# Kernel tuning notes

Hardware: AMD Instinct MI355X
Metric: run time of the kernel (lower is better)

The kernel has to match this reference:

```python
import jax, jax.numpy as jnp
import numpy as np

N_NODES = 50000
N_EDGES = 1600000
IN_DIM = 128
HEADS = 4
HEAD_DIM = 32  # out_dim // heads
N_REL = 3
NEG_SLOPE = 0.2


def setup_inputs() -> dict:
    key = jax.random.key(0)
    ks = jax.random.split(key, 8)
    x = jax.random.normal(ks[0], (N_NODES, IN_DIM), dtype=jnp.float32)
    edge_index = jax.random.randint(ks[1], (2, N_EDGES), 0, N_NODES, dtype=jnp.int64)
    edge_type = jax.random.randint(ks[2], (N_EDGES,), 0, N_REL, dtype=jnp.int64)
    # per-relation GATConv params (PyG layout: lin weight, att_src, att_dst, bias)
    s = 1.0 / np.sqrt(IN_DIM)
    W = jax.random.normal(ks[3], (N_REL, IN_DIM, HEADS * HEAD_DIM), dtype=jnp.float32) * s
    att_src = jax.random.normal(ks[4], (N_REL, HEADS, HEAD_DIM), dtype=jnp.float32) * s
    att_dst = jax.random.normal(ks[5], (N_REL, HEADS, HEAD_DIM), dtype=jnp.float32) * s
    bias = jnp.zeros((N_REL, HEADS * HEAD_DIM), dtype=jnp.float32)
    rel_w = jnp.ones((N_REL,), dtype=jnp.float32)  # relation_weights param
    return {"x": x, "W": W, "att_src": att_src, "att_dst": att_dst,
            "bias": bias, "rel_w": rel_w,
            "edge_index": edge_index, "edge_type": edge_type}


def reference(x, W, att_src, att_dst, bias, rel_w, edge_index, edge_type):
    N = x.shape[0]
    NEG = jnp.float32(-1e9)
    # self loops (GATConv add_self_loops=True) appended; present in every relation
    self_idx = jnp.arange(N, dtype=edge_index.dtype)
    src = jnp.concatenate([edge_index[0], self_idx])  # [E+N]
    dst = jnp.concatenate([edge_index[1], self_idx])  # [E+N]
    weights = jax.nn.softmax(rel_w)
    out = jnp.zeros((N, HEADS * HEAD_DIM), dtype=x.dtype)
    for r in range(N_REL):
        h = (x @ W[r]).reshape(N, HEADS, HEAD_DIM)  # [N,H,C]
        a_s = jnp.einsum('nhc,hc->nh', h, att_src[r])
        a_d = jnp.einsum('nhc,hc->nh', h, att_dst[r])
        score = jax.nn.leaky_relu(a_s[src] + a_d[dst], NEG_SLOPE)  # [E+N,H]
        mask = jnp.concatenate([edge_type == r, jnp.ones((N,), dtype=bool)])
        score = jnp.where(mask[:, None], score, NEG)  # mask out other relations
        # segment softmax over incoming edges per destination node
        smax = jax.ops.segment_max(score, dst, num_segments=N)  # finite: self-loops
        ex = jnp.exp(score - smax[dst])
        denom = jax.ops.segment_sum(ex, dst, num_segments=N)
        alpha = ex / denom[dst]  # [E+N,H]
        msg = alpha[:, :, None] * h[src]  # [E+N,H,C]
        rel_out = jax.ops.segment_sum(msg, dst, num_segments=N).reshape(N, HEADS * HEAD_DIM)
        out = out + weights[r] * (rel_out + bias[r])
    return out
```

## Files before the change

### kernel.cpp

```cpp
#include <hip/hip_runtime.h>
#include <hip/hip_bf16.h>
#include <hip/hip_fp16.h>
#include <math.h>

#define IN_DIM 128
#define OUT_DIM 128
#define HEADS 4
#define HEAD_DIM 32
#define NREL 3
#define NEG_SLOPE 0.2f

#define CHUNK 4096
#define BUCK_SHIFT 7
#define DPB 128
#define KPB 384
#define CAPE 6144
#define CAPS (CAPE + 3*DPB)

typedef __attribute__((ext_vector_type(8))) short short8;
typedef __attribute__((ext_vector_type(4))) float f32x4;
typedef unsigned short u16;

static __device__ __forceinline__ float leaky(float x){ return fmaxf(x, NEG_SLOPE*x); }
static __device__ __forceinline__ unsigned bf16rn(float x){
  unsigned b = __float_as_uint(x);
  b += 0x7FFF + ((b>>16)&1u);
  return b>>16;
}
static __device__ __forceinline__ unsigned h2pack(float a, float b){
  union { __half h[2]; unsigned u; } p;
  p.h[0] = __float2half_rn(a); p.h[1] = __float2half_rn(b);
  return p.u;
}

__global__ __launch_bounds__(256) void k_wprep(
    const float* __restrict__ W, const float* __restrict__ att_s,
    const float* __restrict__ att_d, const float* __restrict__ rw,
    const float* __restrict__ bias, u16* __restrict__ WTall,
    float* __restrict__ smw, float* __restrict__ biasMix){
  const int r = blockIdx.x / 9;
  const int tile = blockIdx.x % 9;
  const int t = threadIdx.x;
  const float* Wr = W + (size_t)r*IN_DIM*OUT_DIM;
  u16* WT = WTall + (size_t)r*144*128;
  if (tile < 8){
    const int col0 = tile*16;
    for (int i=t; i<16*128; i+=256){
      int col = col0 + (i>>7), k = i&127;
      WT[col*128 + k] = (u16)bf16rn(Wr[k*128 + col]);
    }
    return;
  }
  if (t < 128){
    int k = t;
    for (int h=0; h<4; h++){
      float ss=0.f, sd=0.f;
      for (int c=0; c<32; c++){
        float w = Wr[k*128 + h*32 + c];
        ss = fmaf(w, att_s[(r*4+h)*32+c], ss);
        sd = fmaf(w, att_d[(r*4+h)*32+c], sd);
      }
      WT[(128+h)*128 + k] = (u16)bf16rn(ss);
      WT[(132+h)*128 + k] = (u16)bf16rn(sd);
    }
  }
  for (int i=t; i<8*128; i+=256) WT[136*128 + i] = 0;
  if (r == 0){
    float m = fmaxf(rw[0], fmaxf(rw[1], rw[2]));
    float e0=__expf(rw[0]-m), e1=__expf(rw[1]-m), e2=__expf(rw[2]-m);
    float inv = 1.f/(e0+e1+e2);
    if (t < 3) smw[t] = (t==0?e0:(t==1?e1:e2))*inv;
    if (t < 128)
      biasMix[t] = inv*(e0*bias[t] + e1*bias[OUT_DIM+t] + e2*bias[2*OUT_DIM+t]);
  }
}

__global__ __launch_bounds__(256) void k_gemmhist(
    const float* __restrict__ x, const u16* __restrict__ WTall,
    unsigned* __restrict__ hq, float* __restrict__ as_, float* __restrict__ ad_,
    const int* __restrict__ ei, int* __restrict__ histG,
    int N, int E, int NCHUNK, int NBUCK){
  __shared__ int h[512];
  const int t = threadIdx.x;

  if (blockIdx.x < (unsigned)NCHUNK){
    const int c = blockIdx.x;
    h[t] = 0; h[t+256] = 0; __syncthreads();
    const int* dstp = ei + E;
    const int base = c*CHUNK;
    #pragma unroll 4
    for (int it=0; it<CHUNK/256; ++it){
      int e = base + it*256 + t;
      if (e < E) atomicAdd(&h[dstp[e]>>BUCK_SHIFT], 1);
    }
    __syncthreads();
    for (int k=t; k<NBUCK; k+=256) histG[k*NCHUNK + c] = h[k];
    return;
  }

  const int w = t >> 6;
  const int l = t & 63;
  const int row0 = (blockIdx.x - NCHUNK)*128 + w*32;
  const int lg = l >> 4;
  const int lc = l & 15;

  short8 afrag[4][2];
  #pragma unroll
  for (int ks=0; ks<4; ks++){
    const int k0 = ks*32 + lg*8;
    #pragma unroll
    for (int rf=0; rf<2; rf++){
      int row = row0 + rf*16 + lc;
      float4 v0, v1;
      if (row < N){
        const float4* xp = (const float4*)(x + (size_t)row*IN_DIM + k0);
        v0 = xp[0]; v1 = xp[1];
      } else { v0 = float4{0.f,0.f,0.f,0.f}; v1 = v0; }
      union { short8 s; unsigned u[4]; } pa;
      pa.u[0] = bf16rn(v0.x) | (bf16rn(v0.y)<<16);
      pa.u[1] = bf16rn(v0.z) | (bf16rn(v0.w)<<16);
      pa.u[2] = bf16rn(v1.x) | (bf16rn(v1.y)<<16);
      pa.u[3] = bf16rn(v1.z) | (bf16rn(v1.w)<<16);
      afrag[ks][rf] = pa.s;
    }
  }

  for (int r=0; r<NREL; r++){
    const u16* WT = WTall + (size_t)r*144*128;
    f32x4 acc[2][9];
    #pragma unroll
    for (int rf=0; rf<2; rf++)
      #pragma unroll
      for (int cf=0; cf<9; cf++) acc[rf][cf] = (f32x4){0.f,0.f,0.f,0.f};

    #pragma unroll
    for (int ks=0; ks<4; ks++){
      const int k0 = ks*32 + lg*8;
      #pragma unroll
      for (int cf=0; cf<9; cf++){
        short8 b = *(const short8*)(WT + (size_t)(cf*16 + lc)*128 + k0);
        #pragma unroll
        for (int rf=0; rf<2; rf++)
          acc[rf][cf] = __builtin_amdgcn_mfma_f32_16x16x32_bf16(afrag[ks][rf], b, acc[rf][cf], 0, 0, 0);
      }
    }

    #pragma unroll
    for (int rf=0; rf<2; rf++){
      #pragma unroll
      for (int j=0; j<4; j++){
        int row = row0 + rf*16 + lg*4 + j;
        bool ok = (row < N);
        size_t nidx = (size_t)r*N + row;
        #pragma unroll
        for (int cf=0; cf<8; cf++){
          float v = acc[rf][cf][j];
          float pv = __shfl_xor(v, 1);
          if (ok && !(l&1))
            hq[nidx*64 + cf*8 + (lc>>1)] = bf16rn(v) | (bf16rn(pv)<<16);
        }
        float av = acc[rf][8][j];
        if (ok && lc < 4)       as_[nidx*4 + lc]     = av;
        else if (ok && lc < 8)  ad_[nidx*4 + (lc-4)] = av;
      }
    }
  }
}

__global__ __launch_bounds__(256) void k_scanSeg(const int* __restrict__ histG,
                        int* __restrict__ chunkOff, int* __restrict__ totalE, int NCHUNK){
  __shared__ int sh[512];
  __shared__ int ps[256];
  const int b = blockIdx.x, t = threadIdx.x;
  sh[t]     = (t     < NCHUNK) ? histG[b*NCHUNK + t]     : 0;
  sh[t+256] = (t+256 < NCHUNK) ? histG[b*NCHUNK + t+256] : 0;
  __syncthreads();
  int e0 = sh[2*t], pair = e0 + sh[2*t+1];
  ps[t] = pair; __syncthreads();
  int x = pair;
  for (int off=1; off<256; off<<=1){
    int y = (t>=off)?ps[t-off]:0; __syncthreads();
    x += y; ps[t] = x; __syncthreads();
  }
  int ex = x - pair;
  if (2*t   < NCHUNK) chunkOff[b*NCHUNK + 2*t]   = ex;
  if (2*t+1 < NCHUNK) chunkOff[b*NCHUNK + 2*t+1] = ex + e0;
  if (t == 255) totalE[b] = x;
}

__global__ __launch_bounds__(256) void k_part(const int* __restrict__ et, const int* __restrict__ ei,
                       const int* __restrict__ chunkOff, unsigned* __restrict__ payload,
                       int E, int NCHUNK, int NBUCK){
  __shared__ int cur[512];
  const int c = blockIdx.x, t = threadIdx.x;
  for (int k=t; k<NBUCK; k+=256) cur[k] = k*CAPE + chunkOff[k*NCHUNK + c];
  __syncthreads();
  const int* dstp = ei + E;
  const int base = c*CHUNK;
  #pragma unroll 4
  for (int it=0; it<CHUNK/256; ++it){
    int e = base + it*256 + t;
    if (e < E){
      int d = dstp[e];
      int s = ei[e];
      int r = et[e];
      int b = d >> BUCK_SHIFT;
      int pos = atomicAdd(&cur[b], 1);
      payload[pos] = (unsigned)((d & (DPB-1)) | (r<<7) | (s<<9));
    }
  }
}

__global__ __launch_bounds__(512) void k_csr(const unsigned* __restrict__ payload,
                     const int* __restrict__ totalE,
                     const float* __restrict__ as_, const float* __restrict__ ad_,
                     const float* __restrict__ smw,
                     int* __restrict__ offs, uint4* __restrict__ slot,
                     float4* __restrict__ ivg,
                     int E, int N, int NCHUNK, int NBUCK){
  __shared__ int cntA[KPB];
  __shared__ int cur[KPB];
  __shared__ float den[KPB*4];
  __shared__ float4 adl[KPB];
  __shared__ int ps[DPB];
  const int b = blockIdx.x, t = threadIdx.x;
  const int bs = b*CAPE;
  const int be = bs + totalE[b];
  const int outbase = b*CAPS;
  const int validD = min(N - b*DPB, DPB);

  for (int k=t; k<KPB; k+=512) cntA[k] = 0;
  for (int k=t; k<KPB*4; k+=512) den[k] = 0.f;
  for (int k=t; k<KPB; k+=512){
    int dl = k/3, r = k - dl*3;
    int d2 = b*DPB + dl;
    adl[k] = (d2 < N) ? ((const float4*)ad_)[(size_t)r*N + d2] : (float4){0,0,0,0};
  }
  __syncthreads();
  for (int i=bs+t; i<be; i+=512){
    unsigned p = payload[i];
    atomicAdd(&cntA[(int)(p&(DPB-1))*NREL + (int)((p>>7)&3u)], 1);
  }
  __syncthreads();
  const int dst = b*DPB + t;
  int c0=0,c1=0,c2=0,sum=0,o0=0,o1=0,o2=0,hs=0;
  if (t < DPB){
    hs = (dst < N) ? 1 : 0;
    c0 = cntA[3*t]   + hs;
    c1 = cntA[3*t+1] + hs;
    c2 = cntA[3*t+2] + hs;
    sum = c0+c1+c2;
    ps[t] = sum;
  }
  __syncthreads();
  int xsc = sum;
  for (int off=1; off<DPB; off<<=1){
    int y = (t < DPB && t >= off) ? ps[t-off] : 0;
    __syncthreads();
    if (t < DPB) { xsc += y; ps[t] = xsc; }
    __syncthreads();
  }
  if (t < DPB){
    int ex = xsc - sum;
    o0 = outbase + ex; o1 = o0 + c0; o2 = o1 + c1;
    offs[b*(KPB+1) + 3*t]   = o0;
    offs[b*(KPB+1) + 3*t+1] = o1;
    offs[b*(KPB+1) + 3*t+2] = o2;
    cur[3*t]   = (o0 - outbase) + hs;
    cur[3*t+1] = (o1 - outbase) + hs;
    cur[3*t+2] = (o2 - outbase) + hs;
  }
  if (t == 0) offs[b*(KPB+1) + KPB] = outbase + (be - bs) + 3*validD;
  __syncthreads();
  for (int i=bs+t; i<be; i+=512){
    unsigned p = payload[i];
    int dl = (int)(p&(DPB-1)), r = (int)((p>>7)&3u), s = (int)(p>>9);
    int lkey = dl*NREL + r;
    int pos = outbase + atomicAdd(&cur[lkey], 1);
    float4 a4 = ((const float4*)as_)[(size_t)r*N + s];
    float4 b4 = adl[lkey];
    float ex0 = __expf(leaky(a4.x+b4.x));
    float ex1 = __expf(leaky(a4.y+b4.y));
    float ex2 = __expf(leaky(a4.z+b4.z));
    float ex3 = __expf(leaky(a4.w+b4.w));
    slot[pos] = (uint4){ (unsigned)(s | (r<<16)), h2pack(ex0,ex1), h2pack(ex2,ex3), 0u };
    atomicAdd(&den[lkey*4+0], ex0); atomicAdd(&den[lkey*4+1], ex1);
    atomicAdd(&den[lkey*4+2], ex2); atomicAdd(&den[lkey*4+3], ex3);
  }
  __syncthreads();
  if (t < DPB && dst < N){
    int starts[3] = {o0, o1, o2};
    #pragma unroll
    for (int r=0; r<NREL; r++){
      int lkey = 3*t + r;
      float4 a4 = ((const float4*)as_)[(size_t)r*N + dst];
      float4 b4 = adl[lkey];
      float s0 = __expf(leaky(a4.x+b4.x));
      float s1 = __expf(leaky(a4.y+b4.y));
      float s2 = __expf(leaky(a4.z+b4.z));
      float s3 = __expf(leaky(a4.w+b4.w));
      float w = smw[r];
      float4 iv;
      iv.x = w/(den[lkey*4+0]+s0);
      iv.y = w/(den[lkey*4+1]+s1);
      iv.z = w/(den[lkey*4+2]+s2);
      iv.w = w/(den[lkey*4+3]+s3);
      ivg[dst*3 + r] = iv;
      slot[starts[r]] = (uint4){ (unsigned)(dst | (r<<16)), h2pack(s0,s1), h2pack(s2,s3), 0u };
    }
  }
}

__global__ __launch_bounds__(128) void k_segment(
    const int* __restrict__ offs, const uint4* __restrict__ slot,
    const unsigned* __restrict__ hq,
    const float4* __restrict__ ivg, const float* __restrict__ biasMix,
    float* __restrict__ out, int N){
  const int wave = threadIdx.x >> 6;
  const int lane = threadIdx.x & 63;
  const int dst  = blockIdx.x*2 + wave;
  if (dst >= N) return;
  const int g  = lane >> 3;
  const int l8 = lane & 7;
  const int h0 = l8 >> 2;

  const int bb = dst >> BUCK_SHIFT;
  const int lk = (dst & (DPB-1))*3;
  const int* ob = offs + (size_t)bb*(KPB+1);
  int beg = __builtin_amdgcn_readfirstlane(ob[lk]);
  int end = __builtin_amdgcn_readfirstlane(ob[lk+3]);

  float4 v0 = ivg[dst*3+0], v1 = ivg[dst*3+1], v2 = ivg[dst*3+2];
  float iA0 = h0 ? v0.y : v0.x, iB0 = h0 ? v0.w : v0.z;
  float iA1 = h0 ? v1.y : v1.x, iB1 = h0 ? v1.w : v1.z;
  float iA2 = h0 ? v2.y : v2.x, iB2 = h0 ? v2.w : v2.z;

  float acc0[8], acc1[8];
  #pragma unroll
  for (int q=0; q<8; q++){ acc0[q]=0.f; acc1[q]=0.f; }

  for (int i0=beg; i0<end; i0+=16){
    int i = i0 + g;
    int j = i + 8;
    bool vi = (i < end), vj = (j < end);
    uint4 rec1 = {0,0,0,0}, rec2 = {0,0,0,0};
    if (vi) rec1 = slot[i];
    if (vj) rec2 = slot[j];
    uint4 u0a, u1a, u0b, u1b;
    if (vi){
      int s = (int)(rec1.x & 0xFFFFu);
      int r = (int)((rec1.x >> 16) & 3u);
      const uint4* hp = (const uint4*)(hq + ((size_t)r*N + s)*64 + l8*4);
      u0a = hp[0]; u1a = hp[8];
    }
    if (vj){
      int s = (int)(rec2.x & 0xFFFFu);
      int r = (int)((rec2.x >> 16) & 3u);
      const uint4* hp = (const uint4*)(hq + ((size_t)r*N + s)*64 + l8*4);
      u0b = hp[0]; u1b = hp[8];
    }
    if (vi){
      int r = (int)((rec1.x >> 16) & 3u);
      float ivA = (r==0)? iA0 : (r==1)? iA1 : iA2;
      float ivB = (r==0)? iB0 : (r==1)? iB1 : iB2;
      union { unsigned u; __half h[2]; } pa, pb;
      pa.u = rec1.y; pb.u = rec1.z;
      float a0 = __half2float(pa.h[h0]) * ivA;
      float a1 = __half2float(pb.h[h0]) * ivB;
      const unsigned* p0 = (const unsigned*)&u0a;
      const unsigned* p1 = (const unsigned*)&u1a;
      #pragma unroll
      for (int q=0; q<4; q++){
        acc0[2*q]   = fmaf(a0, __uint_as_float(p0[q]<<16),           acc0[2*q]);
        acc0[2*q+1] = fmaf(a0, __uint_as_float(p0[q] & 0xFFFF0000u), acc0[2*q+1]);
        acc1[2*q]   = fmaf(a1, __uint_as_float(p1[q]<<16),           acc1[2*q]);
        acc1[2*q+1] = fmaf(a1, __uint_as_float(p1[q] & 0xFFFF0000u), acc1[2*q+1]);
      }
    }
    if (vj){
      int r = (int)((rec2.x >> 16) & 3u);
      float ivA = (r==0)? iA0 : (r==1)? iA1 : iA2;
      float ivB = (r==0)? iB0 : (r==1)? iB1 : iB2;
      union { unsigned u; __half h[2]; } pa, pb;
      pa.u = rec2.y; pb.u = rec2.z;
      float a0 = __half2float(pa.h[h0]) * ivA;
      float a1 = __half2float(pb.h[h0]) * ivB;
      const unsigned* p0 = (const unsigned*)&u0b;
      const unsigned* p1 = (const unsigned*)&u1b;
      #pragma unroll
      for (int q=0; q<4; q++){
        acc0[2*q]   = fmaf(a0, __uint_as_float(p0[q]<<16),           acc0[2*q]);
        acc0[2*q+1] = fmaf(a0, __uint_as_float(p0[q] & 0xFFFF0000u), acc0[2*q+1]);
        acc1[2*q]   = fmaf(a1, __uint_as_float(p1[q]<<16),           acc1[2*q]);
        acc1[2*q+1] = fmaf(a1, __uint_as_float(p1[q] & 0xFFFF0000u), acc1[2*q+1]);
      }
    }
  }

  #pragma unroll
  for (int o=8; o<=32; o<<=1){
    #pragma unroll
    for (int q=0; q<8; q++){
      acc0[q] += __shfl_xor(acc0[q], o);
      acc1[q] += __shfl_xor(acc1[q], o);
    }
  }

  if (g == 0){
    const float4* bmA = (const float4*)(biasMix + 8*l8);
    const float4* bmB = (const float4*)(biasMix + 64 + 8*l8);
    float4 x0 = bmA[0], x1 = bmA[1], y0 = bmB[0], y1 = bmB[1];
    float* orow = out + (size_t)dst*OUT_DIM;
    float4 o0 = {acc0[0]+x0.x, acc0[1]+x0.y, acc0[2]+x0.z, acc0[3]+x0.w};
    float4 o1 = {acc0[4]+x1.x, acc0[5]+x1.y, acc0[6]+x1.z, acc0[7]+x1.w};
    float4 o2 = {acc1[0]+y0.x, acc1[1]+y0.y, acc1[2]+y0.z, acc1[3]+y0.w};
    float4 o3 = {acc1[4]+y1.x, acc1[5]+y1.y, acc1[6]+y1.z, acc1[7]+y1.w};
    *(float4*)(orow + 8*l8)          = o0;
    *(float4*)(orow + 8*l8 + 4)      = o1;
    *(float4*)(orow + 64 + 8*l8)     = o2;
    *(float4*)(orow + 64 + 8*l8 + 4) = o3;
  }
}

extern "C" void kernel_launch(void* const* d_in, const int* in_sizes, int n_in,
                              void* d_out, int out_size, void* d_ws, size_t ws_size,
                              hipStream_t stream) {
  const float* x     = (const float*)d_in[0];
  const float* W     = (const float*)d_in[1];
  const float* att_s = (const float*)d_in[2];
  const float* att_d = (const float*)d_in[3];
  const float* bias  = (const float*)d_in[4];
  const float* rw    = (const float*)d_in[5];
  const int*   ei    = (const int*)d_in[6];
  const int*   et    = (const int*)d_in[7];
  float* out = (float*)d_out;

  const int N = in_sizes[0] / IN_DIM;
  const int E = in_sizes[7];
  const int M = NREL * N;
  const int NCHUNK = (E + CHUNK - 1) / CHUNK;
  const int NBUCK  = (N + DPB - 1) / DPB;
  const int GB     = (N + 127) / 128;

  char* ws = (char*)d_ws;
  size_t off = 0;
  auto alloc = [&](size_t bytes) -> void* {
    void* p = ws + off; off += (bytes + 255) & ~(size_t)255; return p;
  };
  unsigned* hq       = (unsigned*)alloc((size_t)M * 64 * 4);
  float*    as_      = (float*)   alloc((size_t)M * 4 * 4);
  float*    ad_      = (float*)   alloc((size_t)M * 4 * 4);
  int*      offs     = (int*)     alloc((size_t)NBUCK * (KPB+1) * 4);
  int*      histG    = (int*)     alloc((size_t)NBUCK * NCHUNK * 4);
  int*      chunkOff = (int*)     alloc((size_t)NBUCK * NCHUNK * 4);
  int*      totalE   = (int*)     alloc((size_t)NBUCK * 4);
  unsigned* payload  = (unsigned*)alloc((size_t)NBUCK * CAPE * 4);
  uint4*    slot     = (uint4*)   alloc((size_t)NBUCK * CAPS * 16);
  float4*   ivg      = (float4*)  alloc((size_t)M * 16);
  float*    smw      = (float*)   alloc(256);
  float*    biasMix  = (float*)   alloc(512);
  u16*      WTall    = (u16*)     alloc((size_t)NREL * 144 * 128 * 2);

  k_wprep<<<NREL*9, 256, 0, stream>>>(W, att_s, att_d, rw, bias, WTall, smw, biasMix);
  k_gemmhist<<<NCHUNK + GB, 256, 0, stream>>>(x, WTall, hq, as_, ad_, ei, histG, N, E, NCHUNK, NBUCK);
  k_scanSeg<<<NBUCK, 256, 0, stream>>>(histG, chunkOff, totalE, NCHUNK);
  k_part<<<NCHUNK, 256, 0, stream>>>(et, ei, chunkOff, payload, E, NCHUNK, NBUCK);
  k_csr<<<NBUCK, 512, 0, stream>>>(payload, totalE, as_, ad_, smw, offs, slot, ivg, E, N, NCHUNK, NBUCK);
  k_segment<<<(N + 1) / 2, 128, 0, stream>>>(offs, slot, hq, ivg, biasMix, out, N);
}
```

Baseline: 202.4 us.

## Stage GEMM output in LDS, transpose histogram layout, cache payload in LDS, wave-scan

The GEMM epilogue now writes bf16 results into a shared-memory tile and then stores full 16-byte rows to global memory, replacing scattered 4-byte shuffled stores. The chunk histogram and offset arrays are transposed to chunk-major order so the histogram and partition kernels write and read them contiguously, while the scan kernel now reads with a stride. The CSR kernel keeps the bucket payload in LDS for its second pass instead of reloading it from global, and replaces the barrier-heavy block scan with wave shuffle scans. The larger LDS footprint in the CSR and GEMM kernels may reduce occupancy.

```diff
diff --git a/kernel.cpp b/kernel.cpp
--- a/kernel.cpp
+++ b/kernel.cpp
@@ -80,10 +80,11 @@
     unsigned* __restrict__ hq, float* __restrict__ as_, float* __restrict__ ad_,
     const int* __restrict__ ei, int* __restrict__ histG,
     int N, int E, int NCHUNK, int NBUCK){
-  __shared__ int h[512];
+  __shared__ u16 lds16[128][136];
   const int t = threadIdx.x;
 
   if (blockIdx.x < (unsigned)NCHUNK){
+    int* h = (int*)&lds16[0][0];
     const int c = blockIdx.x;
     h[t] = 0; h[t+256] = 0; __syncthreads();
     const int* dstp = ei + E;
@@ -94,13 +95,14 @@
       if (e < E) atomicAdd(&h[dstp[e]>>BUCK_SHIFT], 1);
     }
     __syncthreads();
-    for (int k=t; k<NBUCK; k+=256) histG[k*NCHUNK + c] = h[k];
+    for (int k=t; k<NBUCK; k+=256) histG[c*NBUCK + k] = h[k];
     return;
   }
 
   const int w = t >> 6;
   const int l = t & 63;
-  const int row0 = (blockIdx.x - NCHUNK)*128 + w*32;
+  const int blkrow0 = (blockIdx.x - NCHUNK)*128;
+  const int row0 = blkrow0 + w*32;
   const int lg = l >> 4;
   const int lc = l & 15;
 
@@ -145,35 +147,46 @@
       }
     }
 
+    __syncthreads();
     #pragma unroll
     for (int rf=0; rf<2; rf++){
       #pragma unroll
       for (int j=0; j<4; j++){
+        const int rloc = w*32 + rf*16 + lg*4 + j;
+        #pragma unroll
+        for (int cf=0; cf<8; cf++)
+          lds16[rloc][cf*16 + lc] = (u16)bf16rn(acc[rf][cf][j]);
         int row = row0 + rf*16 + lg*4 + j;
-        bool ok = (row < N);
-        size_t nidx = (size_t)r*N + row;
-        #pragma unroll
-        for (int cf=0; cf<8; cf++){
-          float v = acc[rf][cf][j];
-          float pv = __shfl_xor(v, 1);
-          if (ok && !(l&1))
-            hq[nidx*64 + cf*8 + (lc>>1)] = bf16rn(v) | (bf16rn(pv)<<16);
+        float av = acc[rf][8][j];
+        if (row < N){
+          size_t nidx = (size_t)r*N + row;
+          if (lc < 4)       as_[nidx*4 + lc]     = av;
+          else if (lc < 8)  ad_[nidx*4 + (lc-4)] = av;
         }
-        float av = acc[rf][8][j];
-        if (ok && lc < 4)       as_[nidx*4 + lc]     = av;
-        else if (ok && lc < 8)  ad_[nidx*4 + (lc-4)] = av;
+      }
+    }
+    __syncthreads();
+    #pragma unroll
+    for (int k=0; k<8; k++){
+      int i = t + 256*k;
+      int row = i >> 4, q = i & 15;
+      int grow = blkrow0 + row;
+      if (grow < N){
+        size_t nidx = (size_t)r*N + grow;
+        *(uint4*)(hq + nidx*64 + q*4) = *(const uint4*)&lds16[row][q*8];
       }
     }
   }
 }
 
 __global__ __launch_bounds__(256) void k_scanSeg(const int* __restrict__ histG,
-                        int* __restrict__ chunkOff, int* __restrict__ totalE, int NCHUNK){
+                        int* __restrict__ chunkOff, int* __restrict__ totalE,
+                        int NCHUNK, int NBUCK){
   __shared__ int sh[512];
   __shared__ int ps[256];
   const int b = blockIdx.x, t = threadIdx.x;
-  sh[t]     = (t     < NCHUNK) ? histG[b*NCHUNK + t]     : 0;
-  sh[t+256] = (t+256 < NCHUNK) ? histG[b*NCHUNK + t+256] : 0;
+  sh[t]     = (t     < NCHUNK) ? histG[(size_t)t*NBUCK + b]       : 0;
+  sh[t+256] = (t+256 < NCHUNK) ? histG[(size_t)(t+256)*NBUCK + b] : 0;
   __syncthreads();
   int e0 = sh[2*t], pair = e0 + sh[2*t+1];
   ps[t] = pair; __syncthreads();
@@ -183,8 +196,8 @@
     x += y; ps[t] = x; __syncthreads();
   }
   int ex = x - pair;
-  if (2*t   < NCHUNK) chunkOff[b*NCHUNK + 2*t]   = ex;
-  if (2*t+1 < NCHUNK) chunkOff[b*NCHUNK + 2*t+1] = ex + e0;
+  if (2*t   < NCHUNK) chunkOff[(size_t)(2*t)*NBUCK + b]   = ex;
+  if (2*t+1 < NCHUNK) chunkOff[(size_t)(2*t+1)*NBUCK + b] = ex + e0;
   if (t == 255) totalE[b] = x;
 }
 
@@ -193,7 +206,7 @@
                        int E, int NCHUNK, int NBUCK){
   __shared__ int cur[512];
   const int c = blockIdx.x, t = threadIdx.x;
-  for (int k=t; k<NBUCK; k+=256) cur[k] = k*CAPE + chunkOff[k*NCHUNK + c];
+  for (int k=t; k<NBUCK; k+=256) cur[k] = k*CAPE + chunkOff[(size_t)c*NBUCK + k];
   __syncthreads();
   const int* dstp = ei + E;
   const int base = c*CHUNK;
@@ -218,14 +231,15 @@
                      int* __restrict__ offs, uint4* __restrict__ slot,
                      float4* __restrict__ ivg,
                      int E, int N, int NCHUNK, int NBUCK){
+  __shared__ unsigned shp[CAPE];
   __shared__ int cntA[KPB];
   __shared__ int cur[KPB];
   __shared__ float den[KPB*4];
   __shared__ float4 adl[KPB];
-  __shared__ int ps[DPB];
+  __shared__ int wtot[2];
   const int b = blockIdx.x, t = threadIdx.x;
   const int bs = b*CAPE;
-  const int be = bs + totalE[b];
+  const int ne = totalE[b];
   const int outbase = b*CAPS;
   const int validD = min(N - b*DPB, DPB);
 
@@ -237,31 +251,31 @@
     adl[k] = (d2 < N) ? ((const float4*)ad_)[(size_t)r*N + d2] : (float4){0,0,0,0};
   }
   __syncthreads();
-  for (int i=bs+t; i<be; i+=512){
-    unsigned p = payload[i];
+  for (int i=t; i<ne; i+=512){
+    unsigned p = payload[bs + i];
+    shp[i] = p;
     atomicAdd(&cntA[(int)(p&(DPB-1))*NREL + (int)((p>>7)&3u)], 1);
   }
   __syncthreads();
   const int dst = b*DPB + t;
-  int c0=0,c1=0,c2=0,sum=0,o0=0,o1=0,o2=0,hs=0;
+  int c0=0,c1=0,c2=0,sum=0,o0=0,o1=0,o2=0,hs=0,xinc=0;
   if (t < DPB){
     hs = (dst < N) ? 1 : 0;
     c0 = cntA[3*t]   + hs;
     c1 = cntA[3*t+1] + hs;
     c2 = cntA[3*t+2] + hs;
     sum = c0+c1+c2;
-    ps[t] = sum;
-  }
-  __syncthreads();
-  int xsc = sum;
-  for (int off=1; off<DPB; off<<=1){
-    int y = (t < DPB && t >= off) ? ps[t-off] : 0;
-    __syncthreads();
-    if (t < DPB) { xsc += y; ps[t] = xsc; }
-    __syncthreads();
-  }
+    xinc = sum;
+    #pragma unroll
+    for (int o=1; o<64; o<<=1){
+      int y = __shfl_up(xinc, o);
+      if ((t & 63) >= o) xinc += y;
+    }
+    if ((t & 63) == 63) wtot[t>>6] = xinc;
+  }
+  __syncthreads();
   if (t < DPB){
-    int ex = xsc - sum;
+    int ex = xinc - sum + ((t >= 64) ? wtot[0] : 0);
     o0 = outbase + ex; o1 = o0 + c0; o2 = o1 + c1;
     offs[b*(KPB+1) + 3*t]   = o0;
     offs[b*(KPB+1) + 3*t+1] = o1;
@@ -270,10 +284,10 @@
     cur[3*t+1] = (o1 - outbase) + hs;
     cur[3*t+2] = (o2 - outbase) + hs;
   }
-  if (t == 0) offs[b*(KPB+1) + KPB] = outbase + (be - bs) + 3*validD;
-  __syncthreads();
-  for (int i=bs+t; i<be; i+=512){
-    unsigned p = payload[i];
+  if (t == 0) offs[b*(KPB+1) + KPB] = outbase + ne + 3*validD;
+  __syncthreads();
+  for (int i=t; i<ne; i+=512){
+    unsigned p = shp[i];
     int dl = (int)(p&(DPB-1)), r = (int)((p>>7)&3u), s = (int)(p>>9);
     int lkey = dl*NREL + r;
     int pos = outbase + atomicAdd(&cur[lkey], 1);
@@ -463,7 +477,7 @@
 
   k_wprep<<<NREL*9, 256, 0, stream>>>(W, att_s, att_d, rw, bias, WTall, smw, biasMix);
   k_gemmhist<<<NCHUNK + GB, 256, 0, stream>>>(x, WTall, hq, as_, ad_, ei, histG, N, E, NCHUNK, NBUCK);
-  k_scanSeg<<<NBUCK, 256, 0, stream>>>(histG, chunkOff, totalE, NCHUNK);
+  k_scanSeg<<<NBUCK, 256, 0, stream>>>(histG, chunkOff, totalE, NCHUNK, NBUCK);
   k_part<<<NCHUNK, 256, 0, stream>>>(et, ei, chunkOff, payload, E, NCHUNK, NBUCK);
   k_csr<<<NBUCK, 512, 0, stream>>>(payload, totalE, as_, ad_, smw, offs, slot, ivg, E, N, NCHUNK, NBUCK);
   k_segment<<<(N + 1) / 2, 128, 0, stream>>>(offs, slot, hq, ivg, biasMix, out, N);
```

New measurement: 200.3 us. About the same (-1.0%).
